# Performance work log

Measured on AMD Instinct MI355X. Metric: run time of the kernel, lower is better.

## Reference

```python
import jax, jax.numpy as jnp
import numpy as np

DIM = 1024
N_HEAD = 16
HEAD_DIM = DIM // N_HEAD
B, T = 4, 2048
NEG = -1e9


def setup_inputs() -> dict:
    key = jax.random.key(0)
    ks = jax.random.split(key, 5)
    x = jax.random.normal(ks[0], (B, T, DIM), dtype=jnp.float32)
    # additive causal mask, broadcast over batch and heads
    causal = jnp.triu(jnp.full((T, T), NEG, dtype=jnp.float32), k=1)
    mask = causal[None, None, :, :]  # [1,1,T,T]
    s = 1.0 / np.sqrt(DIM)
    wq = jax.random.normal(ks[1], (DIM, DIM), dtype=jnp.float32) * s
    wk = jax.random.normal(ks[2], (DIM, DIM), dtype=jnp.float32) * s
    wv = jax.random.normal(ks[3], (DIM, DIM), dtype=jnp.float32) * s
    wo = jax.random.normal(ks[4], (DIM, DIM), dtype=jnp.float32) * s
    return {"x": x, "mask": mask, "wq": wq, "wk": wk, "wv": wv, "wo": wo}


def reference(x, mask, wq, wk, wv, wo):
    Bn, Tn, C = x.shape
    # torch nn.Linear(dim,dim,bias=False): y = x @ W^T
    q = (x @ wq.T).reshape(Bn, Tn, N_HEAD, HEAD_DIM).transpose(0, 2, 1, 3)  # [B,H,T,D]
    k = (x @ wk.T).reshape(Bn, Tn, N_HEAD, HEAD_DIM).transpose(0, 2, 1, 3)
    v = (x @ wv.T).reshape(Bn, Tn, N_HEAD, HEAD_DIM).transpose(0, 2, 1, 3)
    scale = 1.0 / np.sqrt(HEAD_DIM).astype(np.float32)
    attn = jnp.einsum('bhqd,bhkd->bhqk', q, k) * scale  # [B,H,T,T]
    attn = attn + mask
    attn = jax.nn.softmax(attn, axis=-1)
    out = jnp.einsum('bhqk,bhkd->bhqd', attn, v)  # [B,H,T,D]
    out = out.transpose(0, 2, 1, 3).reshape(Bn, Tn, C)
    return out @ wo.T
```

## Files before the change

### kernel.cpp

```cpp
#include <hip/hip_runtime.h>
#include <hip/hip_bf16.h>

typedef __attribute__((ext_vector_type(8))) short short8;
typedef __attribute__((ext_vector_type(4))) short short4v;
typedef __attribute__((ext_vector_type(4))) float float4v;

#define DIM   1024
#define NH    16
#define HD    64
#define BSZ   4
#define TSZ   2048
#define BT    (BSZ*TSZ)

#define PSTR  72

typedef const __attribute__((address_space(1))) void* gptr_t;
typedef __attribute__((address_space(3))) void* lptr_t;

__device__ __forceinline__ short f2bs(float x) {
    __hip_bfloat16 h = __float2bfloat16(x);
    return __builtin_bit_cast(short, h);
}

__global__ __launch_bounds__(256) void cvt_kernel(
    const float* __restrict__ x,  const float* __restrict__ wq,
    const float* __restrict__ wk, const float* __restrict__ wv,
    const float* __restrict__ wo,
    __hip_bfloat16* __restrict__ xb,  __hip_bfloat16* __restrict__ wqb,
    __hip_bfloat16* __restrict__ wkb, __hip_bfloat16* __restrict__ wvb,
    __hip_bfloat16* __restrict__ wob)
{
    int bid = blockIdx.x;
    const float* src; __hip_bfloat16* dst; int base;
    if (bid < 8192) { src = x; dst = xb; base = bid; }
    else {
        int wsel = (bid - 8192) >> 10;
        base = (bid - 8192) & 1023;
        src = (wsel == 0) ? wq : (wsel == 1) ? wk : (wsel == 2) ? wv : wo;
        dst = (wsel == 0) ? wqb : (wsel == 1) ? wkb : (wsel == 2) ? wvb : wob;
    }
    size_t off = (size_t)base * 1024 + threadIdx.x * 4;
    float4v v = *(const float4v*)(src + off);
    short4v o;
    o[0] = f2bs(v[0]); o[1] = f2bs(v[1]); o[2] = f2bs(v[2]); o[3] = f2bs(v[3]);
    *(short4v*)((short*)dst + off) = o;
}

__device__ __forceinline__ void gemm_core(
    const __hip_bfloat16* __restrict__ A,
    const __hip_bfloat16* __restrict__ B,
    __hip_bfloat16* smA, __hip_bfloat16* smB,
    int m0, int n0, int tid, float4v acc[4][4])
{
    const int wid = tid >> 6, lane = tid & 63;
    const int quad = lane >> 4, l15 = lane & 15;
    const int wm = (wid >> 1) * 64, wn = (wid & 1) * 64;
    const int r0 = tid >> 2;
    const int ko = (tid & 3) * 8;

    const __hip_bfloat16* gA0 = A + (size_t)(m0 + r0) * DIM + ko;
    const __hip_bfloat16* gB0 = B + (size_t)(n0 + r0) * DIM + ko;

    for (int kc = 0; kc < DIM; kc += 32) {
        __syncthreads();
        __builtin_amdgcn_global_load_lds((gptr_t)(gA0 + kc),
            (lptr_t)(smA + tid * 8), 16, 0, 0);
        __builtin_amdgcn_global_load_lds((gptr_t)(gA0 + (size_t)64 * DIM + kc),
            (lptr_t)(smA + 2048 + tid * 8), 16, 0, 0);
        __builtin_amdgcn_global_load_lds((gptr_t)(gB0 + kc),
            (lptr_t)(smB + tid * 8), 16, 0, 0);
        __builtin_amdgcn_global_load_lds((gptr_t)(gB0 + (size_t)64 * DIM + kc),
            (lptr_t)(smB + 2048 + tid * 8), 16, 0, 0);
        __syncthreads();

        short8 a[4], b[4];
#pragma unroll
        for (int mb = 0; mb < 4; mb++)
            a[mb] = *(const short8*)(smA + (wm + mb*16 + l15) * 32 + quad * 8);
#pragma unroll
        for (int nb = 0; nb < 4; nb++)
            b[nb] = *(const short8*)(smB + (wn + nb*16 + l15) * 32 + quad * 8);
#pragma unroll
        for (int mb = 0; mb < 4; mb++)
#pragma unroll
            for (int nb = 0; nb < 4; nb++)
                acc[mb][nb] = __builtin_amdgcn_mfma_f32_16x16x32_bf16(
                    a[mb], b[nb], acc[mb][nb], 0, 0, 0);
    }
}

__global__ __launch_bounds__(256) void qkv_gemm(
    const __hip_bfloat16* __restrict__ xb,
    const __hip_bfloat16* __restrict__ wqb,
    const __hip_bfloat16* __restrict__ wkb,
    const __hip_bfloat16* __restrict__ wvb,
    __hip_bfloat16* __restrict__ Qb,
    __hip_bfloat16* __restrict__ Kb,
    __hip_bfloat16* __restrict__ Vt)
{
    __shared__ __hip_bfloat16 smA[128*32];
    __shared__ __hip_bfloat16 smB[128*32];

    const int z = blockIdx.z;
    const __hip_bfloat16* w = (z == 0) ? wqb : ((z == 1) ? wkb : wvb);
    const int tid = threadIdx.x;
    const int wid = tid >> 6, lane = tid & 63;
    const int quad = lane >> 4, l15 = lane & 15;
    const int m0 = blockIdx.x * 128, n0 = blockIdx.y * 128;
    const int wm0 = m0 + (wid >> 1) * 64;
    const int wn0 = n0 + (wid & 1) * 64;
    const float qscale = 0.1803368801111204f;

    float4v acc[4][4];
#pragma unroll
    for (int i = 0; i < 4; i++)
#pragma unroll
        for (int j = 0; j < 4; j++)
#pragma unroll
            for (int r = 0; r < 4; r++) acc[i][j][r] = 0.0f;

    gemm_core(xb, w, smA, smB, m0, n0, tid, acc);

#pragma unroll
    for (int mb = 0; mb < 4; mb++)
#pragma unroll
        for (int nb = 0; nb < 4; nb++)
#pragma unroll
            for (int r = 0; r < 4; r++) {
                int m = wm0 + mb*16 + quad*4 + r;
                int n = wn0 + nb*16 + l15;
                int bb = m >> 11, t = m & 2047;
                int h  = n >> 6,  d = n & 63;
                float v = acc[mb][nb][r];
                if (z == 0)
                    Qb[(size_t)((bb*NH + h)*TSZ + t)*HD + d] = __float2bfloat16(v * qscale);
                else if (z == 1)
                    Kb[(size_t)((bb*NH + h)*TSZ + t)*HD + d] = __float2bfloat16(v);
                else
                    Vt[(size_t)((bb*NH + h)*HD + d)*TSZ + t] = __float2bfloat16(v);
            }
}

__global__ __launch_bounds__(256, 2) void attn(
    const __hip_bfloat16* __restrict__ Qb,
    const __hip_bfloat16* __restrict__ Kb,
    const __hip_bfloat16* __restrict__ Vt,
    __hip_bfloat16* __restrict__ Ob)
{
    __shared__ __hip_bfloat16 smK[64*64];
    __shared__ __hip_bfloat16 smV[64*64];
    __shared__ __hip_bfloat16 Pl[4][32*PSTR];

    const int qperm[16] = {15,14,13,12,8,9,10,11,4,5,6,7,3,2,1,0};
    const int bh = blockIdx.x;
    const int qt = qperm[blockIdx.y];
    const int q0 = qt * 128;
    const int tid = threadIdx.x;
    const int wid = tid >> 6, lane = tid & 63;
    const int quad = lane >> 4, l15 = lane & 15;
    const int l7 = l15 & 7;
    const int q0w = q0 + wid * 32;

    const __hip_bfloat16* Qp = Qb + (size_t)bh * TSZ * HD;
    const __hip_bfloat16* Kp = Kb + (size_t)bh * TSZ * HD;
    const __hip_bfloat16* Vp = Vt + (size_t)bh * HD * TSZ;
    __hip_bfloat16* P = &Pl[wid][0];

    const int srow = tid >> 3;
    const int scol = ((tid & 7) ^ (srow & 7)) * 8;

    short8 bq[2][2];
#pragma unroll
    for (int nt = 0; nt < 2; nt++)
#pragma unroll
        for (int c = 0; c < 2; c++)
            bq[nt][c] = *(const short8*)(Qp + (size_t)(q0w + nt*16 + l15)*HD + c*32 + quad*8);

    float m2[2] = {-1e30f, -1e30f}, lsum[2] = {0.f, 0.f};
    float4v ot[4][2];
#pragma unroll
    for (int mt = 0; mt < 4; mt++)
#pragma unroll
        for (int nt = 0; nt < 2; nt++)
#pragma unroll
            for (int r = 0; r < 4; r++) ot[mt][nt][r] = 0.f;

    const int ntb = 2*qt + 2;
    for (int it = 0; it < ntb; ++it) {
        const int k0 = it * 64;

        __syncthreads();
#pragma unroll
        for (int c = 0; c < 2; c++) {
            __builtin_amdgcn_global_load_lds(
                (gptr_t)(Kp + (size_t)(k0 + srow + 32*c)*HD + scol),
                (lptr_t)(smK + tid*8 + c*2048), 16, 0, 0);
            __builtin_amdgcn_global_load_lds(
                (gptr_t)(Vp + (size_t)(srow + 32*c)*TSZ + k0 + scol),
                (lptr_t)(smV + tid*8 + c*2048), 16, 0, 0);
        }
        __syncthreads();

        if (k0 > q0w + 31) continue;

        float4v st[4][2];
#pragma unroll
        for (int mt = 0; mt < 4; mt++)
#pragma unroll
            for (int nt = 0; nt < 2; nt++)
#pragma unroll
                for (int r = 0; r < 4; r++) st[mt][nt][r] = 0.f;
#pragma unroll
        for (int c = 0; c < 2; c++)
#pragma unroll
            for (int mt = 0; mt < 4; mt++) {
                short8 ak = *(const short8*)(smK + (mt*16 + l15)*64 + ((c*4 + quad) ^ l7)*8);
                st[mt][0] = __builtin_amdgcn_mfma_f32_16x16x32_bf16(ak, bq[0][c], st[mt][0], 0, 0, 0);
                st[mt][1] = __builtin_amdgcn_mfma_f32_16x16x32_bf16(ak, bq[1][c], st[mt][1], 0, 0, 0);
            }

        if (k0 + 63 > q0w) {
#pragma unroll
            for (int mt = 0; mt < 4; mt++)
#pragma unroll
                for (int nt = 0; nt < 2; nt++) {
                    int qn = q0w + nt*16 + l15;
#pragma unroll
                    for (int r = 0; r < 4; r++) {
                        int kg = k0 + mt*16 + quad*4 + r;
                        if (kg > qn) st[mt][nt][r] = -1e30f;
                    }
                }
        }

#pragma unroll
        for (int nt = 0; nt < 2; nt++) {
            float vmax = st[0][nt][0];
#pragma unroll
            for (int mt = 0; mt < 4; mt++)
#pragma unroll
                for (int r = 0; r < 4; r++) vmax = fmaxf(vmax, st[mt][nt][r]);
            vmax = fmaxf(vmax, __shfl_xor(vmax, 16));
            vmax = fmaxf(vmax, __shfl_xor(vmax, 32));

            float mnew = fmaxf(m2[nt], vmax);
            float alpha = exp2f(m2[nt] - mnew);
            m2[nt] = mnew;

            float rs = 0.f;
#pragma unroll
            for (int mt = 0; mt < 4; mt++)
#pragma unroll
                for (int r = 0; r < 4; r++) {
                    float p = exp2f(st[mt][nt][r] - mnew);
                    st[mt][nt][r] = p;
                    rs += p;
                }
            rs += __shfl_xor(rs, 16);
            rs += __shfl_xor(rs, 32);
            lsum[nt] = lsum[nt] * alpha + rs;

#pragma unroll
            for (int mt = 0; mt < 4; mt++)
#pragma unroll
                for (int r = 0; r < 4; r++) ot[mt][nt][r] *= alpha;

#pragma unroll
            for (int mt = 0; mt < 4; mt++) {
                short4v pk;
                pk[0] = f2bs(st[mt][nt][0]); pk[1] = f2bs(st[mt][nt][1]);
                pk[2] = f2bs(st[mt][nt][2]); pk[3] = f2bs(st[mt][nt][3]);
                *(short4v*)(P + (nt*16 + l15)*PSTR + mt*16 + quad*4) = pk;
            }
        }

        short8 bp[2][2];
#pragma unroll
        for (int nt = 0; nt < 2; nt++)
#pragma unroll
            for (int c2 = 0; c2 < 2; c2++)
                bp[nt][c2] = *(const short8*)(P + (nt*16 + l15)*PSTR + c2*32 + quad*8);

#pragma unroll
        for (int c2 = 0; c2 < 2; c2++)
#pragma unroll
            for (int mt = 0; mt < 4; mt++) {
                short8 av = *(const short8*)(smV + (mt*16 + l15)*64 + ((c2*4 + quad) ^ l7)*8);
                ot[mt][0] = __builtin_amdgcn_mfma_f32_16x16x32_bf16(av, bp[0][c2], ot[mt][0], 0, 0, 0);
                ot[mt][1] = __builtin_amdgcn_mfma_f32_16x16x32_bf16(av, bp[1][c2], ot[mt][1], 0, 0, 0);
            }
    }

    const int b = bh >> 4, h = bh & 15;
#pragma unroll
    for (int nt = 0; nt < 2; nt++) {
        const float inv = 1.0f / lsum[nt];
        const int qn = q0w + nt*16 + l15;
        const size_t rowbase = (size_t)((b*TSZ + qn)*NH + h) * HD;
#pragma unroll
        for (int mt = 0; mt < 4; mt++) {
            short4v pk;
            pk[0] = f2bs(ot[mt][nt][0] * inv); pk[1] = f2bs(ot[mt][nt][1] * inv);
            pk[2] = f2bs(ot[mt][nt][2] * inv); pk[3] = f2bs(ot[mt][nt][3] * inv);
            *(short4v*)(Ob + rowbase + mt*16 + quad*4) = pk;
        }
    }
}

__global__ __launch_bounds__(256) void out_gemm(
    const __hip_bfloat16* __restrict__ A,
    const __hip_bfloat16* __restrict__ w,
    float* __restrict__ out)
{
    __shared__ __hip_bfloat16 smA[128*32];
    __shared__ __hip_bfloat16 smB[128*32];

    const int tid = threadIdx.x;
    const int wid = tid >> 6, lane = tid & 63;
    const int quad = lane >> 4, l15 = lane & 15;
    const int m0 = blockIdx.x * 128, n0 = blockIdx.y * 128;
    const int wm0 = m0 + (wid >> 1) * 64;
    const int wn0 = n0 + (wid & 1) * 64;

    float4v acc[4][4];
#pragma unroll
    for (int i = 0; i < 4; i++)
#pragma unroll
        for (int j = 0; j < 4; j++)
#pragma unroll
            for (int r = 0; r < 4; r++) acc[i][j][r] = 0.0f;

    gemm_core(A, w, smA, smB, m0, n0, tid, acc);

#pragma unroll
    for (int mb = 0; mb < 4; mb++)
#pragma unroll
        for (int nb = 0; nb < 4; nb++)
#pragma unroll
            for (int r = 0; r < 4; r++) {
                int m = wm0 + mb*16 + quad*4 + r;
                int n = wn0 + nb*16 + l15;
                out[(size_t)m*DIM + n] = acc[mb][nb][r];
            }
}

extern "C" void kernel_launch(void* const* d_in, const int* in_sizes, int n_in,
                              void* d_out, int out_size, void* d_ws, size_t ws_size,
                              hipStream_t stream) {
    const float* x  = (const float*)d_in[0];
    const float* wq = (const float*)d_in[2];
    const float* wk = (const float*)d_in[3];
    const float* wv = (const float*)d_in[4];
    const float* wo = (const float*)d_in[5];
    float* out = (float*)d_out;

    char* ws = (char*)d_ws;
    const size_t MB = (size_t)1024 * 1024;
    __hip_bfloat16* Qb  = (__hip_bfloat16*)(ws);
    __hip_bfloat16* Kb  = (__hip_bfloat16*)(ws + 16*MB);
    __hip_bfloat16* Vt  = (__hip_bfloat16*)(ws + 32*MB);
    __hip_bfloat16* xb  = (__hip_bfloat16*)(ws + 48*MB);
    __hip_bfloat16* Ob  = (__hip_bfloat16*)(ws + 48*MB);
    __hip_bfloat16* wqb = (__hip_bfloat16*)(ws + 64*MB);
    __hip_bfloat16* wkb = (__hip_bfloat16*)(ws + 66*MB);
    __hip_bfloat16* wvb = (__hip_bfloat16*)(ws + 68*MB);
    __hip_bfloat16* wob = (__hip_bfloat16*)(ws + 70*MB);

    dim3 blk(256);
    cvt_kernel<<<dim3(8192 + 4*1024), blk, 0, stream>>>(
        x, wq, wk, wv, wo, xb, wqb, wkb, wvb, wob);
    qkv_gemm<<<dim3(BT/128, DIM/128, 3), blk, 0, stream>>>(
        xb, wqb, wkb, wvb, Qb, Kb, Vt);
    attn<<<dim3(BSZ*NH, 16), blk, 0, stream>>>(Qb, Kb, Vt, Ob);
    out_gemm<<<dim3(BT/128, DIM/128), blk, 0, stream>>>(Ob, wob, out);
}
```

Before: 284.3 us.

## Widen GEMM K-tile to 64 with XOR-swizzled LDS and vectorized V-transpose stores

The shared GEMM core now stages 64-wide K chunks instead of 32, halving the number of barrier pairs per K loop. It applies an XOR swizzle to the column index when loading into LDS and reading fragments, to avoid bank conflicts on the wider row stride. The QKV epilogue writes the transposed V output as packed 4-element vectors instead of scalar stores. LDS usage doubles per block, which may reduce occupancy.

```diff
diff --git a/kernel.cpp b/kernel.cpp
--- a/kernel.cpp
+++ b/kernel.cpp
@@ -54,38 +54,41 @@
 {
     const int wid = tid >> 6, lane = tid & 63;
     const int quad = lane >> 4, l15 = lane & 15;
+    const int l7 = l15 & 7;
     const int wm = (wid >> 1) * 64, wn = (wid & 1) * 64;
-    const int r0 = tid >> 2;
-    const int ko = (tid & 3) * 8;
-
-    const __hip_bfloat16* gA0 = A + (size_t)(m0 + r0) * DIM + ko;
-    const __hip_bfloat16* gB0 = B + (size_t)(n0 + r0) * DIM + ko;
-
-    for (int kc = 0; kc < DIM; kc += 32) {
+    const int srow = tid >> 3;
+    const int scol = ((tid & 7) ^ (srow & 7)) * 8;
+
+    const __hip_bfloat16* gA0 = A + (size_t)(m0 + srow) * DIM + scol;
+    const __hip_bfloat16* gB0 = B + (size_t)(n0 + srow) * DIM + scol;
+
+    for (int kc = 0; kc < DIM; kc += 64) {
         __syncthreads();
-        __builtin_amdgcn_global_load_lds((gptr_t)(gA0 + kc),
-            (lptr_t)(smA + tid * 8), 16, 0, 0);
-        __builtin_amdgcn_global_load_lds((gptr_t)(gA0 + (size_t)64 * DIM + kc),
-            (lptr_t)(smA + 2048 + tid * 8), 16, 0, 0);
-        __builtin_amdgcn_global_load_lds((gptr_t)(gB0 + kc),
-            (lptr_t)(smB + tid * 8), 16, 0, 0);
-        __builtin_amdgcn_global_load_lds((gptr_t)(gB0 + (size_t)64 * DIM + kc),
-            (lptr_t)(smB + 2048 + tid * 8), 16, 0, 0);
+#pragma unroll
+        for (int j = 0; j < 4; j++) {
+            __builtin_amdgcn_global_load_lds((gptr_t)(gA0 + (size_t)(j*32)*DIM + kc),
+                (lptr_t)(smA + j*2048 + tid*8), 16, 0, 0);
+            __builtin_amdgcn_global_load_lds((gptr_t)(gB0 + (size_t)(j*32)*DIM + kc),
+                (lptr_t)(smB + j*2048 + tid*8), 16, 0, 0);
+        }
         __syncthreads();
 
-        short8 a[4], b[4];
-#pragma unroll
-        for (int mb = 0; mb < 4; mb++)
-            a[mb] = *(const short8*)(smA + (wm + mb*16 + l15) * 32 + quad * 8);
-#pragma unroll
-        for (int nb = 0; nb < 4; nb++)
-            b[nb] = *(const short8*)(smB + (wn + nb*16 + l15) * 32 + quad * 8);
-#pragma unroll
-        for (int mb = 0; mb < 4; mb++)
+#pragma unroll
+        for (int s = 0; s < 2; s++) {
+            short8 a[4], b[4];
+#pragma unroll
+            for (int mb = 0; mb < 4; mb++)
+                a[mb] = *(const short8*)(smA + (wm + mb*16 + l15)*64 + ((s*4 + quad) ^ l7)*8);
 #pragma unroll
             for (int nb = 0; nb < 4; nb++)
-                acc[mb][nb] = __builtin_amdgcn_mfma_f32_16x16x32_bf16(
-                    a[mb], b[nb], acc[mb][nb], 0, 0, 0);
+                b[nb] = *(const short8*)(smB + (wn + nb*16 + l15)*64 + ((s*4 + quad) ^ l7)*8);
+#pragma unroll
+            for (int mb = 0; mb < 4; mb++)
+#pragma unroll
+                for (int nb = 0; nb < 4; nb++)
+                    acc[mb][nb] = __builtin_amdgcn_mfma_f32_16x16x32_bf16(
+                        a[mb], b[nb], acc[mb][nb], 0, 0, 0);
+        }
     }
 }
 
@@ -98,8 +101,8 @@
     __hip_bfloat16* __restrict__ Kb,
     __hip_bfloat16* __restrict__ Vt)
 {
-    __shared__ __hip_bfloat16 smA[128*32];
-    __shared__ __hip_bfloat16 smB[128*32];
+    __shared__ __hip_bfloat16 smA[128*64];
+    __shared__ __hip_bfloat16 smB[128*64];
 
     const int z = blockIdx.z;
     const __hip_bfloat16* w = (z == 0) ? wqb : ((z == 1) ? wkb : wvb);
@@ -121,24 +124,39 @@
 
     gemm_core(xb, w, smA, smB, m0, n0, tid, acc);
 
-#pragma unroll
-    for (int mb = 0; mb < 4; mb++)
-#pragma unroll
-        for (int nb = 0; nb < 4; nb++)
+    if (z == 2) {
+        const int h = wn0 >> 6;
+#pragma unroll
+        for (int mb = 0; mb < 4; mb++) {
+            int m = wm0 + mb*16 + quad*4;
+            int bb = m >> 11, t0 = m & 2047;
+#pragma unroll
+            for (int nb = 0; nb < 4; nb++) {
+                int d = nb*16 + l15;
+                short4v pk;
+                pk[0] = f2bs(acc[mb][nb][0]); pk[1] = f2bs(acc[mb][nb][1]);
+                pk[2] = f2bs(acc[mb][nb][2]); pk[3] = f2bs(acc[mb][nb][3]);
+                *(short4v*)(Vt + (size_t)((bb*NH + h)*HD + d)*TSZ + t0) = pk;
+            }
+        }
+    } else {
+        const float sc = (z == 0) ? qscale : 1.0f;
+        __hip_bfloat16* dst = (z == 0) ? Qb : Kb;
+#pragma unroll
+        for (int mb = 0; mb < 4; mb++)
 #pragma unroll
             for (int r = 0; r < 4; r++) {
                 int m = wm0 + mb*16 + quad*4 + r;
-                int n = wn0 + nb*16 + l15;
                 int bb = m >> 11, t = m & 2047;
-                int h  = n >> 6,  d = n & 63;
-                float v = acc[mb][nb][r];
-                if (z == 0)
-                    Qb[(size_t)((bb*NH + h)*TSZ + t)*HD + d] = __float2bfloat16(v * qscale);
-                else if (z == 1)
-                    Kb[(size_t)((bb*NH + h)*TSZ + t)*HD + d] = __float2bfloat16(v);
-                else
-                    Vt[(size_t)((bb*NH + h)*HD + d)*TSZ + t] = __float2bfloat16(v);
-            }
+#pragma unroll
+                for (int nb = 0; nb < 4; nb++) {
+                    int n = wn0 + nb*16 + l15;
+                    int h = n >> 6, d = n & 63;
+                    dst[(size_t)((bb*NH + h)*TSZ + t)*HD + d] =
+                        __float2bfloat16(acc[mb][nb][r] * sc);
+                }
+            }
+    }
 }
 
 __global__ __launch_bounds__(256, 2) void attn(
@@ -312,8 +330,8 @@
     const __hip_bfloat16* __restrict__ w,
     float* __restrict__ out)
 {
-    __shared__ __hip_bfloat16 smA[128*32];
-    __shared__ __hip_bfloat16 smB[128*32];
+    __shared__ __hip_bfloat16 smA[128*64];
+    __shared__ __hip_bfloat16 smB[128*64];
 
     const int tid = threadIdx.x;
     const int wid = tid >> 6, lane = tid & 63;
```

Result: faster. 261.5 us (-8.0%).
